# Kernel tuning notes

Hardware: AMD Instinct MI355X
Metric: run time of the kernel (lower is better)

## Reference

```python
import jax, jax.numpy as jnp
import numpy as np

N = 20000
E = 320000
IN_DIM = 128
HID = 64
HEADS = 8
OUT_DIM = 128
NEG_SLOPE = 0.2  # PyG GATConv default leaky_relu slope


def _glorot(key, shape):
    fan_in = shape[0] if len(shape) > 1 else shape[-1]
    return jax.random.normal(key, shape, dtype=jnp.float32) / jnp.sqrt(jnp.float32(fan_in))


def setup_inputs() -> dict:
    key = jax.random.key(0)
    ks = jax.random.split(key, 16)
    x = jax.random.normal(ks[0], (N, IN_DIM), dtype=jnp.float32)
    edge_index = jax.random.randint(ks[1], (2, E), 0, N, dtype=jnp.int32)
    HC = HEADS * HID
    return {
        "x": x,
        "edge_index": edge_index,
        # layer 1: in -> heads*hid (concat)
        "W1": _glorot(ks[2], (IN_DIM, HC)),
        "a_src1": _glorot(ks[3], (HEADS, HID)),
        "a_dst1": _glorot(ks[4], (HEADS, HID)),
        "b1": jnp.zeros((HC,), jnp.float32),
        # layer 2: heads*hid -> heads*hid (concat)
        "W2": _glorot(ks[5], (HC, HC)),
        "a_src2": _glorot(ks[6], (HEADS, HID)),
        "a_dst2": _glorot(ks[7], (HEADS, HID)),
        "b2": jnp.zeros((HC,), jnp.float32),
        # layer 3: heads*hid -> out, heads=1, concat=False
        "W3": _glorot(ks[8], (HC, OUT_DIM)),
        "a_src3": _glorot(ks[9], (1, OUT_DIM)),
        "a_dst3": _glorot(ks[10], (1, OUT_DIM)),
        "b3": jnp.zeros((OUT_DIM,), jnp.float32),
    }


def _gat_layer(x, src, dst, W, a_src, a_dst, b, heads, concat):
    # x: [N, F_in] -> h: [N, H, C]
    n = x.shape[0]
    h = (x @ W).reshape(n, heads, -1)
    # per-node attention half-logits: [N, H]
    al_src = jnp.sum(h * a_src[None], axis=-1)
    al_dst = jnp.sum(h * a_dst[None], axis=-1)
    # per-edge logits with leaky relu: [E, H]
    e = jax.nn.leaky_relu(al_src[src] + al_dst[dst], NEG_SLOPE)
    # segment softmax over incoming edges of each dst node
    emax = jax.ops.segment_max(e, dst, num_segments=n)
    ex = jnp.exp(e - emax[dst])
    den = jax.ops.segment_sum(ex, dst, num_segments=n)
    alpha = ex / (den[dst] + 1e-16)
    # weighted scatter-aggregate of source features: [E, H, C] -> [N, H, C]
    out = jax.ops.segment_sum(h[src] * alpha[:, :, None], dst, num_segments=n)
    out = out.reshape(n, -1) if concat else out.mean(axis=1)
    return out + b


def reference(x, edge_index, W1, a_src1, a_dst1, b1, W2, a_src2, a_dst2, b2,
              W3, a_src3, a_dst3, b3):
    # PyG GATConv adds self-loops by default
    loops = jnp.arange(N, dtype=edge_index.dtype)
    src = jnp.concatenate([edge_index[0], loops])
    dst = jnp.concatenate([edge_index[1], loops])
    # eval mode: dropout is identity
    h = _gat_layer(x, src, dst, W1, a_src1, a_dst1, b1, HEADS, True)
    h = jax.nn.elu(h)
    h = _gat_layer(h, src, dst, W2, a_src2, a_dst2, b2, HEADS, True)
    h = jax.nn.elu(h)
    out = _gat_layer(h, src, dst, W3, a_src3, a_dst3, b3, 1, False)
    return out
```

## Files before the change

### kernel.cpp

```cpp
#include <hip/hip_runtime.h>
#include <math.h>

#define NN 20000
#define EE 320000
#define ETOT 340000
#define NHEADS 8
#define HID 64
#define HCV 512
#define IND 128
#define OUTD 128
#define NEG_SLOPE 0.2f

typedef __attribute__((ext_vector_type(8))) _Float16 half8;
typedef __attribute__((ext_vector_type(4))) _Float16 half4;
typedef __attribute__((ext_vector_type(4))) float floatx4;

__device__ __forceinline__ void cvt_one(const float* W, _Float16* T, int idx, int K, int N) {
    int k = idx / N, n = idx - k * N;
    T[(size_t)n * K + k] = (_Float16)W[idx];
}

#define S1 (IND * HCV)
#define S2 (HCV * HCV)
#define S3 (HCV * OUTD)
#define STOT (S1 + S2 + S3)
#define XTOT (NN * IND)
__global__ void prep_kernel(const float* __restrict__ W1, const float* __restrict__ W2,
                            const float* __restrict__ W3, const float* __restrict__ x,
                            const float* __restrict__ as1, const float* __restrict__ ad1,
                            _Float16* __restrict__ T1, _Float16* __restrict__ T2,
                            _Float16* __restrict__ T3, _Float16* __restrict__ xh,
                            float* __restrict__ w1p, int* __restrict__ cnt) {
    int idx = blockIdx.x * blockDim.x + threadIdx.x;
    if (idx < S1) cvt_one(W1, T1, idx, IND, HCV);
    else if (idx < S1 + S2) cvt_one(W2, T2, idx - S1, HCV, HCV);
    else if (idx < STOT) cvt_one(W3, T3, idx - S1 - S2, HCV, OUTD);
    else if (idx < STOT + NN) cnt[idx - STOT] = 0;
    else if (idx < STOT + NN + XTOT) {
        int j = idx - STOT - NN;
        xh[j] = (_Float16)x[j];
    } else if (idx < STOT + NN + XTOT + IND * 16) {
        int j = idx - STOT - NN - XTOT;
        int c = j >> 4, o = j & 15;
        int hh = o & 7;
        const float* av = (o < 8) ? as1 : ad1;
        float s = 0.f;
        #pragma unroll 8
        for (int jj = 0; jj < HID; jj++)
            s = fmaf(W1[c * HCV + hh * HID + jj], av[hh * HID + jj], s);
        w1p[c * 16 + o] = s;
    }
}


__global__ void count_kernel(const int* __restrict__ ei, int* __restrict__ cnt) {
    int i = blockIdx.x * blockDim.x + threadIdx.x;
    if (i >= ETOT) return;
    int v = (i < EE) ? ei[EE + i] : (i - EE);
    atomicAdd(&cnt[v], 1);
}

#define SCH 20
__global__ __launch_bounds__(1024) void scan_kernel(const int* __restrict__ cnt,
                                                    int* __restrict__ row_ptr,
                                                    int* __restrict__ cursor) {
    __shared__ int wtot[16];
    __shared__ int woff[16];
    int t = threadIdx.x;
    int lane = t & 63;
    int wid = t >> 6;
    int base = t * SCH;
    int vals[SCH];
    int s = 0;
    #pragma unroll
    for (int i = 0; i < SCH; i++) {
        int idx = base + i;
        int v = (idx < NN) ? cnt[idx] : 0;
        vals[i] = v;
        s += v;
    }
    int incl = s;
    #pragma unroll
    for (int off = 1; off < 64; off <<= 1) {
        int u = __shfl_up(incl, off);
        if (lane >= off) incl += u;
    }
    int excl = incl - s;
    if (lane == 63) wtot[wid] = incl;
    __syncthreads();
    if (t == 0) {
        int run = 0;
        #pragma unroll
        for (int j = 0; j < 16; j++) { woff[j] = run; run += wtot[j]; }
        row_ptr[NN] = run;
    }
    __syncthreads();
    int run = woff[wid] + excl;
    #pragma unroll
    for (int i = 0; i < SCH; i++) {
        int idx = base + i;
        if (idx < NN) { row_ptr[idx] = run; cursor[idx] = run; run += vals[i]; }
    }
}

__global__ void fill_kernel(const int* __restrict__ ei, int* __restrict__ cursor,
                            int* __restrict__ csr_src) {
    int i = blockIdx.x * blockDim.x + threadIdx.x;
    if (i >= ETOT) return;
    int u, v;
    if (i < EE) { u = ei[i]; v = ei[EE + i]; }
    else        { u = i - EE; v = i - EE; }
    int pos = atomicAdd(&cursor[v], 1);
    csr_src[pos] = u;
}

__global__ void al1_thin(const float* __restrict__ x, const float* __restrict__ w1p,
                         float* __restrict__ als, float* __restrict__ ald) {
    int gid = blockIdx.x * blockDim.x + threadIdx.x;
    int node = gid >> 4, o = gid & 15;
    if (node >= NN) return;
    const float* xr = x + (size_t)node * IND;
    float s = 0.f;
    #pragma unroll 4
    for (int c = 0; c < IND; c++)
        s = fmaf(xr[c], w1p[c * 16 + o], s);
    if (o < 8) als[node * 8 + o] = s;
    else       ald[node * 8 + (o - 8)] = s;
}

__global__ __launch_bounds__(256) void gather1_kernel(const _Float16* __restrict__ xh,
                                                      const int* __restrict__ row_ptr,
                                                      const int* __restrict__ csr_src,
                                                      const float* __restrict__ als,
                                                      const float* __restrict__ ald,
                                                      _Float16* __restrict__ xagg) {
    int lane = threadIdx.x & 63;
    int v = blockIdx.x * 4 + (threadIdx.x >> 6);
    if (v >= NN) return;
    int hd = lane >> 3;
    int cg = lane & 7;
    float adst = ald[v * NHEADS + hd];
    int s0 = row_ptr[v], s1 = row_ptr[v + 1];
    float acc[16] = {};
    float l = 0.f;
    int i = s0;
    for (; i + 4 <= s1; i += 4) {
        int u[4]; float p[4];
        #pragma unroll
        for (int e = 0; e < 4; e++) u[e] = csr_src[i + e];
        #pragma unroll
        for (int e = 0; e < 4; e++) {
            float t = als[u[e] * NHEADS + hd] + adst;
            t = (t > 0.f) ? t : NEG_SLOPE * t;
            p[e] = __expf(fminf(t, 80.f));
        }
        half8 a[4], b[4];
        #pragma unroll
        for (int e = 0; e < 4; e++) {
            a[e] = *(const half8*)&xh[(size_t)u[e] * IND + cg * 16];
            b[e] = *(const half8*)&xh[(size_t)u[e] * IND + cg * 16 + 8];
        }
        #pragma unroll
        for (int e = 0; e < 4; e++) {
            l += p[e];
            #pragma unroll
            for (int j = 0; j < 8; j++) {
                acc[j]     = fmaf(p[e], (float)a[e][j], acc[j]);
                acc[j + 8] = fmaf(p[e], (float)b[e][j], acc[j + 8]);
            }
        }
    }
    for (; i < s1; i++) {
        int u0 = csr_src[i];
        float t0 = als[u0 * NHEADS + hd] + adst;
        t0 = (t0 > 0.f) ? t0 : NEG_SLOPE * t0;
        float p0 = __expf(fminf(t0, 80.f));
        half8 a0 = *(const half8*)&xh[(size_t)u0 * IND + cg * 16];
        half8 b0 = *(const half8*)&xh[(size_t)u0 * IND + cg * 16 + 8];
        l += p0;
        #pragma unroll
        for (int j = 0; j < 8; j++) {
            acc[j]     = fmaf(p0, (float)a0[j], acc[j]);
            acc[j + 8] = fmaf(p0, (float)b0[j], acc[j + 8]);
        }
    }
    float inv = 1.f / (l + 1e-16f);
    half8 o0, o1;
    #pragma unroll
    for (int j = 0; j < 8; j++) {
        o0[j] = (_Float16)(acc[j] * inv);
        o1[j] = (_Float16)(acc[j + 8] * inv);
    }
    size_t base = (size_t)v * (NHEADS * IND) + hd * IND + cg * 16;
    *(half8*)&xagg[base] = o0;
    *(half8*)&xagg[base + 8] = o1;
}

#define LDK 40
__global__ __launch_bounds__(256) void gemm1_bd(const _Float16* __restrict__ xagg,
                                                const _Float16* __restrict__ Bt,
                                                const float* __restrict__ bias,
                                                _Float16* __restrict__ gact,
                                                int M) {
    __shared__ _Float16 sA[64 * LDK];
    __shared__ _Float16 sB[64 * LDK];
    int tid = threadIdx.x;
    int lane = tid & 63;
    int wv = tid >> 6;
    int m0 = blockIdx.x * 64;
    int h = blockIdx.y;
    int quad = lane >> 4;
    int l15 = lane & 15;
    int arow = tid >> 2;
    int ac4 = tid & 3;

    floatx4 acc[4] = {};

    for (int k0 = 0; k0 < IND; k0 += 32) {
        {
            int gm = m0 + arow;
            int4 va;
            if (gm < M) va = *(const int4*)&xagg[(size_t)gm * (NHEADS * IND) + h * IND + k0 + ac4 * 8];
            else        va = make_int4(0, 0, 0, 0);
            *(int4*)&sA[arow * LDK + ac4 * 8] = va;
            int gn = h * 64 + arow;
            int4 vb = *(const int4*)&Bt[(size_t)gn * IND + k0 + ac4 * 8];
            *(int4*)&sB[arow * LDK + ac4 * 8] = vb;
        }
        __syncthreads();
        half8 a[4], b;
        #pragma unroll
        for (int i = 0; i < 4; i++)
            a[i] = *(const half8*)&sA[(i * 16 + l15) * LDK + quad * 8];
        b = *(const half8*)&sB[(wv * 16 + l15) * LDK + quad * 8];
        #pragma unroll
        for (int i = 0; i < 4; i++)
            acc[i] = __builtin_amdgcn_mfma_f32_16x16x32_f16(a[i], b, acc[i], 0, 0, 0);
        __syncthreads();
    }
    #pragma unroll
    for (int i = 0; i < 4; i++) {
        #pragma unroll
        for (int r = 0; r < 4; r++) {
            int gm = m0 + i * 16 + quad * 4 + r;
            if (gm < M) {
                int col = h * 64 + wv * 16 + l15;
                float o = acc[i][r] + bias[col];
                o = (o > 0.f) ? o : (__expf(o) - 1.f);
                gact[(size_t)gm * HCV + col] = (_Float16)o;
            }
        }
    }
}

__global__ __launch_bounds__(256) void gemm_l2(const _Float16* __restrict__ A,
                                               const _Float16* __restrict__ Bt,
                                               _Float16* __restrict__ C16,
                                               const float* __restrict__ a_src,
                                               const float* __restrict__ a_dst,
                                               float* __restrict__ als2,
                                               float* __restrict__ ald2,
                                               int M, int K) {
    __shared__ _Float16 sA[64 * LDK];
    __shared__ _Float16 sB[128 * LDK];
    __shared__ float psum_s[4][64];
    __shared__ float psum_d[4][64];
    int tid = threadIdx.x;
    int lane = tid & 63;
    int wv = tid >> 6;
    int m0 = blockIdx.x * 64, n0 = blockIdx.y * 128;
    int quad = lane >> 4;
    int l15 = lane & 15;
    int arow = tid >> 2;
    int ac4 = tid & 3;

    floatx4 acc[4][2] = {};

    for (int k0 = 0; k0 < K; k0 += 32) {
        {
            int gm = m0 + arow;
            int4 va;
            if (gm < M) va = *(const int4*)&A[(size_t)gm * K + k0 + ac4 * 8];
            else        va = make_int4(0, 0, 0, 0);
            *(int4*)&sA[arow * LDK + ac4 * 8] = va;
            #pragma unroll
            for (int r = 0; r < 2; r++) {
                int gn = n0 + arow + r * 64;
                int4 vb = *(const int4*)&Bt[(size_t)gn * K + k0 + ac4 * 8];
                *(int4*)&sB[(arow + r * 64) * LDK + ac4 * 8] = vb;
            }
        }
        __syncthreads();
        half8 a[4], b[2];
        #pragma unroll
        for (int i = 0; i < 4; i++)
            a[i] = *(const half8*)&sA[(i * 16 + l15) * LDK + quad * 8];
        #pragma unroll
        for (int j = 0; j < 2; j++)
            b[j] = *(const half8*)&sB[(wv * 32 + j * 16 + l15) * LDK + quad * 8];
        #pragma unroll
        for (int i = 0; i < 4; i++)
            #pragma unroll
            for (int j = 0; j < 2; j++)
                acc[i][j] = __builtin_amdgcn_mfma_f32_16x16x32_f16(a[i], b[j], acc[i][j], 0, 0, 0);
        __syncthreads();
    }
    #pragma unroll
    for (int i = 0; i < 4; i++) {
        #pragma unroll
        for (int r = 0; r < 4; r++) {
            int gm = m0 + i * 16 + quad * 4 + r;
            if (gm < M) {
                #pragma unroll
                for (int j = 0; j < 2; j++)
                    C16[(size_t)gm * HCV + n0 + wv * 32 + j * 16 + l15] = (_Float16)acc[i][j][r];
            }
        }
    }
    int h0 = n0 >> 6;
    float as_v[2], ad_v[2];
    #pragma unroll
    for (int j = 0; j < 2; j++) {
        int dim = (wv * 32 + j * 16 + l15) & 63;
        int hh = h0 + (wv >> 1);
        as_v[j] = a_src[hh * HID + dim];
        ad_v[j] = a_dst[hh * HID + dim];
    }
    #pragma unroll
    for (int i = 0; i < 4; i++) {
        #pragma unroll
        for (int r = 0; r < 4; r++) {
            float ps = acc[i][0][r] * as_v[0] + acc[i][1][r] * as_v[1];
            float pd = acc[i][0][r] * ad_v[0] + acc[i][1][r] * ad_v[1];
            #pragma unroll
            for (int off = 1; off <= 8; off <<= 1) {
                ps += __shfl_xor(ps, off);
                pd += __shfl_xor(pd, off);
            }
            if (l15 == 0) {
                int row = i * 16 + quad * 4 + r;
                psum_s[wv][row] = ps;
                psum_d[wv][row] = pd;
            }
        }
    }
    __syncthreads();
    if (tid < 64) {
        int gm = m0 + tid;
        if (gm < M) {
            als2[(size_t)h0 * NN + gm]       = psum_s[0][tid] + psum_s[1][tid];
            als2[(size_t)(h0 + 1) * NN + gm] = psum_s[2][tid] + psum_s[3][tid];
            ald2[(size_t)h0 * NN + gm]       = psum_d[0][tid] + psum_d[1][tid];
            ald2[(size_t)(h0 + 1) * NN + gm] = psum_d[2][tid] + psum_d[3][tid];
        }
    }
}

__global__ __launch_bounds__(256) void gemm3(const _Float16* __restrict__ A,
                                             const _Float16* __restrict__ Bt,
                                             _Float16* __restrict__ C16,
                                             const float* __restrict__ a_src,
                                             const float* __restrict__ a_dst,
                                             float* __restrict__ als,
                                             float* __restrict__ ald,
                                             int M, int K) {
    __shared__ _Float16 sA[64 * LDK];
    __shared__ _Float16 sB[128 * LDK];
    __shared__ float psum_s[4][64];
    __shared__ float psum_d[4][64];
    int tid = threadIdx.x;
    int lane = tid & 63;
    int wv = tid >> 6;
    int m0 = blockIdx.x * 64;
    int quad = lane >> 4;
    int l15 = lane & 15;
    int arow = tid >> 2;
    int ac4 = tid & 3;

    floatx4 acc[4][2] = {};

    for (int k0 = 0; k0 < K; k0 += 32) {
        {
            int gm = m0 + arow;
            int4 va;
            if (gm < M) va = *(const int4*)&A[(size_t)gm * K + k0 + ac4 * 8];
            else        va = make_int4(0, 0, 0, 0);
            *(int4*)&sA[arow * LDK + ac4 * 8] = va;
            #pragma unroll
            for (int r = 0; r < 2; r++) {
                int gn = arow + r * 64;
                int4 vb = *(const int4*)&Bt[(size_t)gn * K + k0 + ac4 * 8];
                *(int4*)&sB[(arow + r * 64) * LDK + ac4 * 8] = vb;
            }
        }
        __syncthreads();
        half8 a[4], b[2];
        #pragma unroll
        for (int i = 0; i < 4; i++)
            a[i] = *(const half8*)&sA[(i * 16 + l15) * LDK + quad * 8];
        #pragma unroll
        for (int j = 0; j < 2; j++)
            b[j] = *(const half8*)&sB[(wv * 32 + j * 16 + l15) * LDK + quad * 8];
        #pragma unroll
        for (int i = 0; i < 4; i++)
            #pragma unroll
            for (int j = 0; j < 2; j++)
                acc[i][j] = __builtin_amdgcn_mfma_f32_16x16x32_f16(a[i], b[j], acc[i][j], 0, 0, 0);
        __syncthreads();
    }
    #pragma unroll
    for (int i = 0; i < 4; i++) {
        #pragma unroll
        for (int r = 0; r < 4; r++) {
            int gm = m0 + i * 16 + quad * 4 + r;
            if (gm < M) {
                #pragma unroll
                for (int j = 0; j < 2; j++)
                    C16[(size_t)gm * OUTD + wv * 32 + j * 16 + l15] = (_Float16)acc[i][j][r];
            }
        }
    }
    float as_v[2], ad_v[2];
    #pragma unroll
    for (int j = 0; j < 2; j++) {
        as_v[j] = a_src[wv * 32 + j * 16 + l15];
        ad_v[j] = a_dst[wv * 32 + j * 16 + l15];
    }
    #pragma unroll
    for (int i = 0; i < 4; i++) {
        #pragma unroll
        for (int r = 0; r < 4; r++) {
            float ps = acc[i][0][r] * as_v[0] + acc[i][1][r] * as_v[1];
            float pd = acc[i][0][r] * ad_v[0] + acc[i][1][r] * ad_v[1];
            #pragma unroll
            for (int off = 1; off <= 8; off <<= 1) {
                ps += __shfl_xor(ps, off);
                pd += __shfl_xor(pd, off);
            }
            if (l15 == 0) {
                int row = i * 16 + quad * 4 + r;
                psum_s[wv][row] = ps;
                psum_d[wv][row] = pd;
            }
        }
    }
    __syncthreads();
    if (tid < 64) {
        int gm = m0 + tid;
        if (gm < M) {
            als[gm] = psum_s[0][tid] + psum_s[1][tid] + psum_s[2][tid] + psum_s[3][tid];
            ald[gm] = psum_d[0][tid] + psum_d[1][tid] + psum_d[2][tid] + psum_d[3][tid];
        }
    }
}

__global__ __launch_bounds__(256) void gather2_kernel(const _Float16* __restrict__ h,
                                                      const int* __restrict__ row_ptr,
                                                      const int* __restrict__ csr_src,
                                                      const float* __restrict__ als2,
                                                      const float* __restrict__ ald2,
                                                      const float* __restrict__ bias,
                                                      _Float16* __restrict__ gout) {
    int tid = threadIdx.x;
    int lane = tid & 63;
    int wid = tid >> 6;
    int bid = blockIdx.x;
    int hd = bid & 7;
    int sub = lane >> 3;
    int dl = lane & 7;
    int v = (bid >> 3) * 32 + wid * 8 + sub;
    if (v >= NN) return;
    const float* asl = als2 + (size_t)hd * NN;
    float adst = ald2[(size_t)hd * NN + v];
    int s0 = row_ptr[v], s1 = row_ptr[v + 1];
    const _Float16* hh = h + hd * HID + dl * 8;
    float acc[8] = {};
    float l = 0.f;
    int j = s0;
    for (; j + 2 <= s1; j += 2) {
        int u0 = csr_src[j];
        int u1 = csr_src[j + 1];
        half8 x0 = *(const half8*)&hh[(size_t)u0 * HCV];
        half8 x1 = *(const half8*)&hh[(size_t)u1 * HCV];
        float t0 = asl[u0] + adst;
        float t1 = asl[u1] + adst;
        t0 = (t0 > 0.f) ? t0 : NEG_SLOPE * t0;
        t1 = (t1 > 0.f) ? t1 : NEG_SLOPE * t1;
        float p0 = __expf(fminf(t0, 80.f));
        float p1 = __expf(fminf(t1, 80.f));
        l += p0 + p1;
        #pragma unroll
        for (int k = 0; k < 8; k++) {
            acc[k] = fmaf(p0, (float)x0[k], acc[k]);
            acc[k] = fmaf(p1, (float)x1[k], acc[k]);
        }
    }
    if (j < s1) {
        int u0 = csr_src[j];
        half8 x0 = *(const half8*)&hh[(size_t)u0 * HCV];
        float t0 = asl[u0] + adst;
        t0 = (t0 > 0.f) ? t0 : NEG_SLOPE * t0;
        float p0 = __expf(fminf(t0, 80.f));
        l += p0;
        #pragma unroll
        for (int k = 0; k < 8; k++)
            acc[k] = fmaf(p0, (float)x0[k], acc[k]);
    }
    float inv = 1.f / (l + 1e-16f);
    half8 hv;
    #pragma unroll
    for (int k = 0; k < 8; k++) {
        float o = fmaf(acc[k], inv, bias[hd * HID + dl * 8 + k]);
        o = (o > 0.f) ? o : (__expf(o) - 1.f);
        hv[k] = (_Float16)o;
    }
    half8* dst = (half8*)&gout[(size_t)v * HCV + hd * HID + dl * 8];
    __builtin_nontemporal_store(hv, dst);
}

__global__ __launch_bounds__(256) void gather3_kernel(const _Float16* __restrict__ h,
                                                      const int* __restrict__ row_ptr,
                                                      const int* __restrict__ csr_src,
                                                      const float* __restrict__ als,
                                                      const float* __restrict__ ald,
                                                      const float* __restrict__ bias,
                                                      float* __restrict__ out) {
    int lane = threadIdx.x & 63;
    int v = blockIdx.x * 4 + (threadIdx.x >> 6);
    if (v >= NN) return;
    int e_sub = lane >> 4;
    int cg = lane & 15;
    float adst = ald[v];
    int s0 = row_ptr[v], s1 = row_ptr[v + 1];
    float m = -INFINITY;
    for (int i = s0 + e_sub; i < s1; i += 4) {
        int u = csr_src[i];
        float t = als[u] + adst;
        t = (t > 0.f) ? t : NEG_SLOPE * t;
        m = fmaxf(m, t);
    }
    m = fmaxf(m, __shfl_xor(m, 16));
    m = fmaxf(m, __shfl_xor(m, 32));
    float acc[8] = {};
    float l = 0.f;
    for (int i = s0 + e_sub; i < s1; i += 4) {
        int u = csr_src[i];
        float t = als[u] + adst;
        t = (t > 0.f) ? t : NEG_SLOPE * t;
        float p = __expf(t - m);
        half8 x = *(const half8*)&h[(size_t)u * OUTD + cg * 8];
        l += p;
        #pragma unroll
        for (int j = 0; j < 8; j++)
            acc[j] = fmaf(p, (float)x[j], acc[j]);
    }
    l += __shfl_xor(l, 16);
    l += __shfl_xor(l, 32);
    #pragma unroll
    for (int j = 0; j < 8; j++) {
        acc[j] += __shfl_xor(acc[j], 16);
        acc[j] += __shfl_xor(acc[j], 32);
    }
    if (e_sub == 0) {
        float inv = 1.f / (l + 1e-16f);
        float4 o0, o1;
        o0.x = fmaf(acc[0], inv, bias[cg * 8 + 0]);
        o0.y = fmaf(acc[1], inv, bias[cg * 8 + 1]);
        o0.z = fmaf(acc[2], inv, bias[cg * 8 + 2]);
        o0.w = fmaf(acc[3], inv, bias[cg * 8 + 3]);
        o1.x = fmaf(acc[4], inv, bias[cg * 8 + 4]);
        o1.y = fmaf(acc[5], inv, bias[cg * 8 + 5]);
        o1.z = fmaf(acc[6], inv, bias[cg * 8 + 6]);
        o1.w = fmaf(acc[7], inv, bias[cg * 8 + 7]);
        *(float4*)&out[(size_t)v * OUTD + cg * 8] = o0;
        *(float4*)&out[(size_t)v * OUTD + cg * 8 + 4] = o1;
    }
}


extern "C" void kernel_launch(void* const* d_in, const int* in_sizes, int n_in,
                              void* d_out, int out_size, void* d_ws, size_t ws_size,
                              hipStream_t stream) {
    const float* x     = (const float*)d_in[0];
    const int*   ei    = (const int*)d_in[1];
    const float* W1    = (const float*)d_in[2];
    const float* as1   = (const float*)d_in[3];
    const float* ad1   = (const float*)d_in[4];
    const float* b1    = (const float*)d_in[5];
    const float* W2    = (const float*)d_in[6];
    const float* as2   = (const float*)d_in[7];
    const float* ad2   = (const float*)d_in[8];
    const float* b2    = (const float*)d_in[9];
    const float* W3    = (const float*)d_in[10];
    const float* as3   = (const float*)d_in[11];
    const float* ad3   = (const float*)d_in[12];
    const float* b3    = (const float*)d_in[13];
    float* out = (float*)d_out;

    size_t off = 0;
    auto carve = [&](size_t bytes) {
        void* p = (char*)d_ws + off;
        off += (bytes + 255) & ~(size_t)255;
        return p;
    };
    int* row_ptr   = (int*)carve((NN + 1) * sizeof(int));
    int* cursor    = (int*)carve(NN * sizeof(int));
    int* csr_src   = (int*)carve(ETOT * sizeof(int));
    _Float16* xh   = (_Float16*)carve((size_t)NN * IND * sizeof(_Float16));
    _Float16* xagg = (_Float16*)carve((size_t)NN * NHEADS * IND * sizeof(_Float16));
    _Float16* gact = (_Float16*)carve((size_t)NN * HCV * sizeof(_Float16));
    _Float16* hf16 = (_Float16*)carve((size_t)NN * HCV * sizeof(_Float16));
    _Float16* h3   = (_Float16*)carve((size_t)NN * OUTD * sizeof(_Float16));
    float* als     = (float*)carve((size_t)NN * NHEADS * sizeof(float));
    float* ald     = (float*)carve((size_t)NN * NHEADS * sizeof(float));
    float* als2    = (float*)carve((size_t)NN * NHEADS * sizeof(float));
    float* ald2    = (float*)carve((size_t)NN * NHEADS * sizeof(float));
    float* w1p     = (float*)carve((size_t)IND * 16 * sizeof(float));
    _Float16* W1T  = (_Float16*)carve((size_t)S1 * sizeof(_Float16));
    _Float16* W2T  = (_Float16*)carve((size_t)S2 * sizeof(_Float16));
    _Float16* W3T  = (_Float16*)carve((size_t)S3 * sizeof(_Float16));
    _Float16* gact2 = xagg;
    (void)ws_size; (void)n_in; (void)in_sizes; (void)out_size;

    dim3 blk(256);

    int prep_n = STOT + NN + XTOT + IND * 16;
    prep_kernel<<<(prep_n + 255) / 256, blk, 0, stream>>>(W1, W2, W3, x, as1, ad1,
        W1T, W2T, W3T, xh, w1p, cursor);

    count_kernel<<<(ETOT + 255) / 256, blk, 0, stream>>>(ei, cursor);
    scan_kernel<<<1, 1024, 0, stream>>>(cursor, row_ptr, cursor);
    fill_kernel<<<(ETOT + 255) / 256, blk, 0, stream>>>(ei, cursor, csr_src);

    int mt64 = (NN + 63) / 64;
    int nwaves_n = (NN + 3) / 4;

    al1_thin<<<(NN * 16 + 255) / 256, blk, 0, stream>>>(x, w1p, als, ald);
    gather1_kernel<<<nwaves_n, blk, 0, stream>>>(xh, row_ptr, csr_src, als, ald, xagg);
    gemm1_bd<<<dim3(mt64, NHEADS), blk, 0, stream>>>(xagg, W1T, b1, gact, NN);

    gemm_l2<<<dim3(mt64, HCV / 128), blk, 0, stream>>>(gact, W2T, hf16, as2, ad2, als2, ald2, NN, HCV);
    int nb2 = (NN + 31) / 32;
    gather2_kernel<<<dim3(nb2 * 8), blk, 0, stream>>>(hf16, row_ptr, csr_src, als2, ald2, b2, gact2);

    gemm3<<<dim3(mt64, 1), blk, 0, stream>>>(gact2, W3T, h3, as3, ad3, als, ald, NN, HCV);
    gather3_kernel<<<nwaves_n, blk, 0, stream>>>(h3, row_ptr, csr_src, als, ald, b3, out);
}
```

Measured before the change: 332.2 us.

## Reorder layer 1 to project before aggregation, reusing layer-2 GEMM and gather kernels

```diff
diff --git a/kernel.cpp b/kernel.cpp
--- a/kernel.cpp
+++ b/kernel.cpp
@@ -12,7 +12,6 @@
 #define NEG_SLOPE 0.2f
 
 typedef __attribute__((ext_vector_type(8))) _Float16 half8;
-typedef __attribute__((ext_vector_type(4))) _Float16 half4;
 typedef __attribute__((ext_vector_type(4))) float floatx4;
 
 __device__ __forceinline__ void cvt_one(const float* W, _Float16* T, int idx, int K, int N) {
@@ -27,10 +26,9 @@
 #define XTOT (NN * IND)
 __global__ void prep_kernel(const float* __restrict__ W1, const float* __restrict__ W2,
                             const float* __restrict__ W3, const float* __restrict__ x,
-                            const float* __restrict__ as1, const float* __restrict__ ad1,
                             _Float16* __restrict__ T1, _Float16* __restrict__ T2,
                             _Float16* __restrict__ T3, _Float16* __restrict__ xh,
-                            float* __restrict__ w1p, int* __restrict__ cnt) {
+                            int* __restrict__ cnt) {
     int idx = blockIdx.x * blockDim.x + threadIdx.x;
     if (idx < S1) cvt_one(W1, T1, idx, IND, HCV);
     else if (idx < S1 + S2) cvt_one(W2, T2, idx - S1, HCV, HCV);
@@ -39,16 +37,6 @@
     else if (idx < STOT + NN + XTOT) {
         int j = idx - STOT - NN;
         xh[j] = (_Float16)x[j];
-    } else if (idx < STOT + NN + XTOT + IND * 16) {
-        int j = idx - STOT - NN - XTOT;
-        int c = j >> 4, o = j & 15;
-        int hh = o & 7;
-        const float* av = (o < 8) ? as1 : ad1;
-        float s = 0.f;
-        #pragma unroll 8
-        for (int jj = 0; jj < HID; jj++)
-            s = fmaf(W1[c * HCV + hh * HID + jj], av[hh * HID + jj], s);
-        w1p[c * 16 + o] = s;
     }
 }
 
@@ -114,146 +102,8 @@
     csr_src[pos] = u;
 }
 
-__global__ void al1_thin(const float* __restrict__ x, const float* __restrict__ w1p,
-                         float* __restrict__ als, float* __restrict__ ald) {
-    int gid = blockIdx.x * blockDim.x + threadIdx.x;
-    int node = gid >> 4, o = gid & 15;
-    if (node >= NN) return;
-    const float* xr = x + (size_t)node * IND;
-    float s = 0.f;
-    #pragma unroll 4
-    for (int c = 0; c < IND; c++)
-        s = fmaf(xr[c], w1p[c * 16 + o], s);
-    if (o < 8) als[node * 8 + o] = s;
-    else       ald[node * 8 + (o - 8)] = s;
-}
-
-__global__ __launch_bounds__(256) void gather1_kernel(const _Float16* __restrict__ xh,
-                                                      const int* __restrict__ row_ptr,
-                                                      const int* __restrict__ csr_src,
-                                                      const float* __restrict__ als,
-                                                      const float* __restrict__ ald,
-                                                      _Float16* __restrict__ xagg) {
-    int lane = threadIdx.x & 63;
-    int v = blockIdx.x * 4 + (threadIdx.x >> 6);
-    if (v >= NN) return;
-    int hd = lane >> 3;
-    int cg = lane & 7;
-    float adst = ald[v * NHEADS + hd];
-    int s0 = row_ptr[v], s1 = row_ptr[v + 1];
-    float acc[16] = {};
-    float l = 0.f;
-    int i = s0;
-    for (; i + 4 <= s1; i += 4) {
-        int u[4]; float p[4];
-        #pragma unroll
-        for (int e = 0; e < 4; e++) u[e] = csr_src[i + e];
-        #pragma unroll
-        for (int e = 0; e < 4; e++) {
-            float t = als[u[e] * NHEADS + hd] + adst;
-            t = (t > 0.f) ? t : NEG_SLOPE * t;
-            p[e] = __expf(fminf(t, 80.f));
-        }
-        half8 a[4], b[4];
-        #pragma unroll
-        for (int e = 0; e < 4; e++) {
-            a[e] = *(const half8*)&xh[(size_t)u[e] * IND + cg * 16];
-            b[e] = *(const half8*)&xh[(size_t)u[e] * IND + cg * 16 + 8];
-        }
-        #pragma unroll
-        for (int e = 0; e < 4; e++) {
-            l += p[e];
-            #pragma unroll
-            for (int j = 0; j < 8; j++) {
-                acc[j]     = fmaf(p[e], (float)a[e][j], acc[j]);
-                acc[j + 8] = fmaf(p[e], (float)b[e][j], acc[j + 8]);
-            }
-        }
-    }
-    for (; i < s1; i++) {
-        int u0 = csr_src[i];
-        float t0 = als[u0 * NHEADS + hd] + adst;
-        t0 = (t0 > 0.f) ? t0 : NEG_SLOPE * t0;
-        float p0 = __expf(fminf(t0, 80.f));
-        half8 a0 = *(const half8*)&xh[(size_t)u0 * IND + cg * 16];
-        half8 b0 = *(const half8*)&xh[(size_t)u0 * IND + cg * 16 + 8];
-        l += p0;
-        #pragma unroll
-        for (int j = 0; j < 8; j++) {
-            acc[j]     = fmaf(p0, (float)a0[j], acc[j]);
-            acc[j + 8] = fmaf(p0, (float)b0[j], acc[j + 8]);
-        }
-    }
-    float inv = 1.f / (l + 1e-16f);
-    half8 o0, o1;
-    #pragma unroll
-    for (int j = 0; j < 8; j++) {
-        o0[j] = (_Float16)(acc[j] * inv);
-        o1[j] = (_Float16)(acc[j + 8] * inv);
-    }
-    size_t base = (size_t)v * (NHEADS * IND) + hd * IND + cg * 16;
-    *(half8*)&xagg[base] = o0;
-    *(half8*)&xagg[base + 8] = o1;
-}
-
 #define LDK 40
-__global__ __launch_bounds__(256) void gemm1_bd(const _Float16* __restrict__ xagg,
-                                                const _Float16* __restrict__ Bt,
-                                                const float* __restrict__ bias,
-                                                _Float16* __restrict__ gact,
-                                                int M) {
-    __shared__ _Float16 sA[64 * LDK];
-    __shared__ _Float16 sB[64 * LDK];
-    int tid = threadIdx.x;
-    int lane = tid & 63;
-    int wv = tid >> 6;
-    int m0 = blockIdx.x * 64;
-    int h = blockIdx.y;
-    int quad = lane >> 4;
-    int l15 = lane & 15;
-    int arow = tid >> 2;
-    int ac4 = tid & 3;
-
-    floatx4 acc[4] = {};
-
-    for (int k0 = 0; k0 < IND; k0 += 32) {
-        {
-            int gm = m0 + arow;
-            int4 va;
-            if (gm < M) va = *(const int4*)&xagg[(size_t)gm * (NHEADS * IND) + h * IND + k0 + ac4 * 8];
-            else        va = make_int4(0, 0, 0, 0);
-            *(int4*)&sA[arow * LDK + ac4 * 8] = va;
-            int gn = h * 64 + arow;
-            int4 vb = *(const int4*)&Bt[(size_t)gn * IND + k0 + ac4 * 8];
-            *(int4*)&sB[arow * LDK + ac4 * 8] = vb;
-        }
-        __syncthreads();
-        half8 a[4], b;
-        #pragma unroll
-        for (int i = 0; i < 4; i++)
-            a[i] = *(const half8*)&sA[(i * 16 + l15) * LDK + quad * 8];
-        b = *(const half8*)&sB[(wv * 16 + l15) * LDK + quad * 8];
-        #pragma unroll
-        for (int i = 0; i < 4; i++)
-            acc[i] = __builtin_amdgcn_mfma_f32_16x16x32_f16(a[i], b, acc[i], 0, 0, 0);
-        __syncthreads();
-    }
-    #pragma unroll
-    for (int i = 0; i < 4; i++) {
-        #pragma unroll
-        for (int r = 0; r < 4; r++) {
-            int gm = m0 + i * 16 + quad * 4 + r;
-            if (gm < M) {
-                int col = h * 64 + wv * 16 + l15;
-                float o = acc[i][r] + bias[col];
-                o = (o > 0.f) ? o : (__expf(o) - 1.f);
-                gact[(size_t)gm * HCV + col] = (_Float16)o;
-            }
-        }
-    }
-}
-
-__global__ __launch_bounds__(256) void gemm_l2(const _Float16* __restrict__ A,
+__global__ __launch_bounds__(256) void gemm_al(const _Float16* __restrict__ A,
                                                const _Float16* __restrict__ Bt,
                                                _Float16* __restrict__ C16,
                                                const float* __restrict__ a_src,
@@ -454,13 +304,13 @@
     }
 }
 
-__global__ __launch_bounds__(256) void gather2_kernel(const _Float16* __restrict__ h,
-                                                      const int* __restrict__ row_ptr,
-                                                      const int* __restrict__ csr_src,
-                                                      const float* __restrict__ als2,
-                                                      const float* __restrict__ ald2,
-                                                      const float* __restrict__ bias,
-                                                      _Float16* __restrict__ gout) {
+__global__ __launch_bounds__(256) void gather_kernel(const _Float16* __restrict__ h,
+                                                     const int* __restrict__ row_ptr,
+                                                     const int* __restrict__ csr_src,
+                                                     const float* __restrict__ als2,
+                                                     const float* __restrict__ ald2,
+                                                     const float* __restrict__ bias,
+                                                     _Float16* __restrict__ gout) {
     int tid = threadIdx.x;
     int lane = tid & 63;
     int wid = tid >> 6;
@@ -477,25 +327,27 @@
     float acc[8] = {};
     float l = 0.f;
     int j = s0;
-    for (; j + 2 <= s1; j += 2) {
-        int u0 = csr_src[j];
-        int u1 = csr_src[j + 1];
-        half8 x0 = *(const half8*)&hh[(size_t)u0 * HCV];
-        half8 x1 = *(const half8*)&hh[(size_t)u1 * HCV];
-        float t0 = asl[u0] + adst;
-        float t1 = asl[u1] + adst;
-        t0 = (t0 > 0.f) ? t0 : NEG_SLOPE * t0;
-        t1 = (t1 > 0.f) ? t1 : NEG_SLOPE * t1;
-        float p0 = __expf(fminf(t0, 80.f));
-        float p1 = __expf(fminf(t1, 80.f));
-        l += p0 + p1;
-        #pragma unroll
-        for (int k = 0; k < 8; k++) {
-            acc[k] = fmaf(p0, (float)x0[k], acc[k]);
-            acc[k] = fmaf(p1, (float)x1[k], acc[k]);
-        }
-    }
-    if (j < s1) {
+    for (; j + 4 <= s1; j += 4) {
+        int u[4]; float p[4]; half8 xv[4];
+        #pragma unroll
+        for (int e = 0; e < 4; e++) u[e] = csr_src[j + e];
+        #pragma unroll
+        for (int e = 0; e < 4; e++) xv[e] = *(const half8*)&hh[(size_t)u[e] * HCV];
+        #pragma unroll
+        for (int e = 0; e < 4; e++) {
+            float t = asl[u[e]] + adst;
+            t = (t > 0.f) ? t : NEG_SLOPE * t;
+            p[e] = __expf(fminf(t, 80.f));
+        }
+        #pragma unroll
+        for (int e = 0; e < 4; e++) {
+            l += p[e];
+            #pragma unroll
+            for (int k = 0; k < 8; k++)
+                acc[k] = fmaf(p[e], (float)xv[e][k], acc[k]);
+        }
+    }
+    for (; j < s1; j++) {
         int u0 = csr_src[j];
         half8 x0 = *(const half8*)&hh[(size_t)u0 * HCV];
         float t0 = asl[u0] + adst;
@@ -607,26 +459,23 @@
     int* cursor    = (int*)carve(NN * sizeof(int));
     int* csr_src   = (int*)carve(ETOT * sizeof(int));
     _Float16* xh   = (_Float16*)carve((size_t)NN * IND * sizeof(_Float16));
-    _Float16* xagg = (_Float16*)carve((size_t)NN * NHEADS * IND * sizeof(_Float16));
+    _Float16* h1   = (_Float16*)carve((size_t)NN * HCV * sizeof(_Float16));
     _Float16* gact = (_Float16*)carve((size_t)NN * HCV * sizeof(_Float16));
     _Float16* hf16 = (_Float16*)carve((size_t)NN * HCV * sizeof(_Float16));
     _Float16* h3   = (_Float16*)carve((size_t)NN * OUTD * sizeof(_Float16));
     float* als     = (float*)carve((size_t)NN * NHEADS * sizeof(float));
     float* ald     = (float*)carve((size_t)NN * NHEADS * sizeof(float));
-    float* als2    = (float*)carve((size_t)NN * NHEADS * sizeof(float));
-    float* ald2    = (float*)carve((size_t)NN * NHEADS * sizeof(float));
-    float* w1p     = (float*)carve((size_t)IND * 16 * sizeof(float));
     _Float16* W1T  = (_Float16*)carve((size_t)S1 * sizeof(_Float16));
     _Float16* W2T  = (_Float16*)carve((size_t)S2 * sizeof(_Float16));
     _Float16* W3T  = (_Float16*)carve((size_t)S3 * sizeof(_Float16));
-    _Float16* gact2 = xagg;
+    _Float16* gact2 = h1;
     (void)ws_size; (void)n_in; (void)in_sizes; (void)out_size;
 
     dim3 blk(256);
 
-    int prep_n = STOT + NN + XTOT + IND * 16;
-    prep_kernel<<<(prep_n + 255) / 256, blk, 0, stream>>>(W1, W2, W3, x, as1, ad1,
-        W1T, W2T, W3T, xh, w1p, cursor);
+    int prep_n = STOT + NN + XTOT;
+    prep_kernel<<<(prep_n + 255) / 256, blk, 0, stream>>>(W1, W2, W3, x,
+        W1T, W2T, W3T, xh, cursor);
 
     count_kernel<<<(ETOT + 255) / 256, blk, 0, stream>>>(ei, cursor);
     scan_kernel<<<1, 1024, 0, stream>>>(cursor, row_ptr, cursor);
@@ -634,14 +483,13 @@
 
     int mt64 = (NN + 63) / 64;
     int nwaves_n = (NN + 3) / 4;
-
-    al1_thin<<<(NN * 16 + 255) / 256, blk, 0, stream>>>(x, w1p, als, ald);
-    gather1_kernel<<<nwaves_n, blk, 0, stream>>>(xh, row_ptr, csr_src, als, ald, xagg);
-    gemm1_bd<<<dim3(mt64, NHEADS), blk, 0, stream>>>(xagg, W1T, b1, gact, NN);
-
-    gemm_l2<<<dim3(mt64, HCV / 128), blk, 0, stream>>>(gact, W2T, hf16, as2, ad2, als2, ald2, NN, HCV);
-    int nb2 = (NN + 31) / 32;
-    gather2_kernel<<<dim3(nb2 * 8), blk, 0, stream>>>(hf16, row_ptr, csr_src, als2, ald2, b2, gact2);
+    int nb = (NN + 31) / 32;
+
+    gemm_al<<<dim3(mt64, HCV / 128), blk, 0, stream>>>(xh, W1T, h1, as1, ad1, als, ald, NN, IND);
+    gather_kernel<<<dim3(nb * 8), blk, 0, stream>>>(h1, row_ptr, csr_src, als, ald, b1, gact);
+
+    gemm_al<<<dim3(mt64, HCV / 128), blk, 0, stream>>>(gact, W2T, hf16, as2, ad2, als, ald, NN, HCV);
+    gather_kernel<<<dim3(nb * 8), blk, 0, stream>>>(hf16, row_ptr, csr_src, als, ald, b2, gact2);
 
     gemm3<<<dim3(mt64, 1), blk, 0, stream>>>(gact2, W3T, h3, as3, ad3, als, ald, NN, HCV);
     gather3_kernel<<<nwaves_n, blk, 0, stream>>>(h3, row_ptr, csr_src, als, ald, b3, out);
```

Result: faster. 314.4 us (-5.3%).
